# Performance work log

Measured on AMD Instinct MI355X. Metric: run time of the kernel, lower is better.

Reference implementation:

```python
import jax, jax.numpy as jnp
import numpy as np
from jax import lax

ALPHA = 1.0
BETA = 2.0
NUM_ANTS = 16384
NUM_NODES = 512
BATCH = 4096


def setup_inputs() -> dict:
    key = jax.random.key(0)
    k1, k2, k3 = jax.random.split(key, 3)
    x = jax.random.normal(k1, (BATCH, NUM_NODES), dtype=jnp.float32)
    # matches nn.Parameter(torch.ones(N,N)*0.1)
    pheromone_trails = jnp.ones((NUM_NODES, NUM_NODES), dtype=jnp.float32) * 0.1
    # matches nn.Parameter(torch.rand(N,N)*0.1)
    heuristic_info = jax.random.uniform(k2, (NUM_NODES, NUM_NODES), dtype=jnp.float32) * 0.1
    # matches register_buffer('ant_positions', randint(0, N, (num_ants,)))
    ant_positions = jax.random.randint(k3, (NUM_ANTS,), 0, NUM_NODES, dtype=jnp.int32)
    return {"x": x, "pheromone_trails": pheromone_trails,
            "heuristic_info": heuristic_info, "ant_positions": ant_positions}


def reference(x, pheromone_trails, heuristic_info, ant_positions):
    A, N = NUM_ANTS, NUM_NODES
    ant_ids = jnp.arange(A)

    # NOTE: the torch code's select_next_node always reads the row of the ant's
    # *initial* position (self.ant_positions is never updated inside forward),
    # so the unmasked scores are constant per ant. We replicate that faithfully.
    base = (pheromone_trails[ant_positions] ** ALPHA) * \
           (heuristic_info[ant_positions] ** BETA)          # [A, N]

    visited0 = jnp.zeros((A, N), dtype=bool).at[ant_ids, ant_positions].set(True)
    plen0 = jnp.zeros((A,), dtype=jnp.float32)

    def step(carry, _):
        key, visited, current, plen = carry
        key, sub = jax.random.split(key)
        # torch sets masked entries to 0 (NOT -inf) before softmax; replicate.
        logits = jnp.where(visited, 0.0, base)               # [A, N]
        # categorical == multinomial(softmax(logits), 1), vectorized over ants
        nxt = jax.random.categorical(sub, logits, axis=-1)   # [A] int
        plen = plen + heuristic_info[current, nxt]
        visited = visited.at[ant_ids, nxt].set(True)
        return (key, visited, nxt, plen), nxt

    carry0 = (jax.random.key(42), visited0, ant_positions.astype(jnp.int32), plen0)
    (_, _, _, path_lengths), sampled = lax.scan(step, carry0, None, length=N - 1)

    # full paths: [A, N] = start node followed by N-1 sampled nodes
    paths = jnp.concatenate([ant_positions[:, None].astype(sampled.dtype),
                             sampled.T], axis=1)
    # sequential 'if path_length < best' with strict < keeps the FIRST minimum,
    # which is exactly jnp.argmin
    best_idx = jnp.argmin(path_lengths)
    best_path = paths[best_idx].astype(jnp.float32)          # [N]
    return jnp.broadcast_to(best_path[None, :], (x.shape[0], N))
```

## Files before the change

### kernel.cpp

```cpp
#include <hip/hip_runtime.h>
#include <cstdint>
#include <cstddef>

#define A_NUM_ANTS   16384
#define N_NODES      512
#define N_STEPS      511
#define N_BATCH      4096

constexpr uint32_t rotl32(uint32_t x, int r) { return (x << r) | (x >> (32 - r)); }

constexpr void tf2x32(uint32_t k0, uint32_t k1, uint32_t x0, uint32_t x1,
                      uint32_t& o0, uint32_t& o1) {
  const uint32_t k2 = k0 ^ k1 ^ 0x1BD11BDAu;
  x0 += k0; x1 += k1;
  x0 += x1; x1 = rotl32(x1, 13); x1 ^= x0;
  x0 += x1; x1 = rotl32(x1, 15); x1 ^= x0;
  x0 += x1; x1 = rotl32(x1, 26); x1 ^= x0;
  x0 += x1; x1 = rotl32(x1,  6); x1 ^= x0;
  x0 += k1; x1 += k2 + 1u;
  x0 += x1; x1 = rotl32(x1, 17); x1 ^= x0;
  x0 += x1; x1 = rotl32(x1, 29); x1 ^= x0;
  x0 += x1; x1 = rotl32(x1, 16); x1 ^= x0;
  x0 += x1; x1 = rotl32(x1, 24); x1 ^= x0;
  x0 += k2; x1 += k0 + 2u;
  x0 += x1; x1 = rotl32(x1, 13); x1 ^= x0;
  x0 += x1; x1 = rotl32(x1, 15); x1 ^= x0;
  x0 += x1; x1 = rotl32(x1, 26); x1 ^= x0;
  x0 += x1; x1 = rotl32(x1,  6); x1 ^= x0;
  x0 += k0; x1 += k1 + 3u;
  x0 += x1; x1 = rotl32(x1, 17); x1 ^= x0;
  x0 += x1; x1 = rotl32(x1, 29); x1 ^= x0;
  x0 += x1; x1 = rotl32(x1, 16); x1 ^= x0;
  x0 += x1; x1 = rotl32(x1, 24); x1 ^= x0;
  x0 += k1; x1 += k2 + 4u;
  x0 += x1; x1 = rotl32(x1, 13); x1 ^= x0;
  x0 += x1; x1 = rotl32(x1, 15); x1 ^= x0;
  x0 += x1; x1 = rotl32(x1, 26); x1 ^= x0;
  x0 += x1; x1 = rotl32(x1,  6); x1 ^= x0;
  x0 += k2; x1 += k0 + 5u;
  o0 = x0; o1 = x1;
}

struct Subkeys { uint32_t k0[N_STEPS]; uint32_t k1[N_STEPS]; };

constexpr Subkeys make_subkeys() {
  Subkeys s{};
  uint32_t c0 = 0u, c1 = 42u;
  for (int t = 0; t < N_STEPS; ++t) {
    uint32_t n0 = 0, n1 = 0, s0 = 0, s1 = 0;
    tf2x32(c0, c1, 0u, 0u, n0, n1);
    tf2x32(c0, c1, 0u, 1u, s0, s1);
    s.k0[t] = s0; s.k1[t] = s1;
    c0 = n0; c1 = n1;
  }
  return s;
}

namespace { constexpr Subkeys H_SUBKEYS = make_subkeys(); }
__device__ __constant__ Subkeys SUBKEYS = H_SUBKEYS;

#define NEG_LN2   (-0.69314718056f)

template <bool WRITE_PATH>
__device__ __forceinline__ void simulate_ant(
    int a, int lane,
    const float* __restrict__ pher,
    const float* __restrict__ heur,
    int pos,
    float* __restrict__ plen_out,
    float* __restrict__ path_out)
{
  float    lm[8];
  uint32_t visited = 0;
  float    ebmin, ebmax;
  {
    const float* hrow = heur + (size_t)pos * N_NODES;
    const float* prow = pher + (size_t)pos * N_NODES;
    ebmin = 1.0f; ebmax = 1.0f;
#pragma unroll
    for (int q = 0; q < 8; ++q) {
      const int n = lane * 8 + q;
      const float hv = hrow[n];
      const float base = prow[n] * (hv * hv);
      const float eb = expf(-base);
      lm[q] = NEG_LN2 * eb;
      ebmin = fminf(ebmin, eb);
      ebmax = fmaxf(ebmax, eb);
      if (n == pos) visited |= (1u << q);
    }
  }

  int baddr[6];
#pragma unroll
  for (int r = 0; r < 6; ++r) baddr[r] = ((lane ^ (1 << r)) << 2);

#pragma unroll
  for (int r = 0; r < 6; ++r) {
    ebmin = fminf(ebmin, __int_as_float(
        __builtin_amdgcn_ds_bpermute(baddr[r], __float_as_int(ebmin))));
    ebmax = fmaxf(ebmax, __int_as_float(
        __builtin_amdgcn_ds_bpermute(baddr[r], __float_as_int(ebmax))));
  }
  const float allow = (ebmax / ebmin) * (1.0f + 2e-4f);

  int   cur  = pos;
  float plen = 0.0f;
  if (WRITE_PATH && lane == 0) path_out[0] = (float)pos;

  const uint32_t ctr_base = (uint32_t)(a * N_NODES + lane * 8);

  for (int t = 0; t < N_STEPS; ++t) {
    const uint32_t k0 = SUBKEYS.k0[t];
    const uint32_t k1 = SUBKEYS.k1[t];

    uint32_t m[8];
#pragma unroll
    for (int q = 0; q < 8; ++q) {
      uint32_t o0, o1;
      tf2x32(k0, k1, 0u, ctr_base + (uint32_t)q, o0, o1);
      m[q] = (o0 ^ o1) >> 9;
    }
    uint32_t mmax = m[0];
#pragma unroll
    for (int q = 1; q < 8; ++q) mmax = mmax > m[q] ? mmax : m[q];
#pragma unroll
    for (int r = 0; r < 6; ++r) {
      const uint32_t o = (uint32_t)__builtin_amdgcn_ds_bpermute(baddr[r], (int)mmax);
      mmax = mmax > o ? mmax : o;
    }
    const float L    = 23.0f - __log2f((float)mmax);
    const float uthr = __builtin_amdgcn_exp2f(-L * allow);
    const uint32_t mthr = (uint32_t)(uthr * 8388608.0f * (1.0f - 1e-4f));

    unsigned long long b[8];
    int tot = 0;
#pragma unroll
    for (int q = 0; q < 8; ++q) {
      b[q] = __ballot(m[q] >= mthr);
      tot += __popcll(b[q]);
    }

    int bn;
    if (tot == 1) {
      bn = 0;
#pragma unroll
      for (int q = 0; q < 8; ++q)
        if (b[q]) bn = (int)__builtin_ctzll(b[q]) * 8 + q;
    } else {
      float s[8];
#pragma unroll
      for (int q = 0; q < 8; ++q) {
        const float f  = __uint_as_float(m[q] | 0x3f800000u) - 1.0f;
        const float le = ((visited >> q) & 1u) ? NEG_LN2 : lm[q];
        s[q] = __log2f(f) * le;
      }
      float smin = s[0];
#pragma unroll
      for (int q = 1; q < 8; ++q) smin = fminf(smin, s[q]);
#pragma unroll
      for (int r = 0; r < 6; ++r)
        smin = fminf(smin, __int_as_float(
            __builtin_amdgcn_ds_bpermute(baddr[r], __float_as_int(smin))));
      int fq = 8;
#pragma unroll
      for (int q = 7; q >= 0; --q) if (s[q] == smin) fq = q;
      const unsigned long long mask = __ballot(fq < 8);
      const int winlane = __builtin_ctzll(mask);
      bn = __shfl(fq, winlane, 64) + winlane * 8;
    }

    if ((bn >> 3) == lane) visited |= (1u << (bn & 7));

    plen += heur[(size_t)cur * N_NODES + bn];
    cur = bn;
    if (WRITE_PATH && lane == 0) path_out[t + 1] = (float)bn;
  }

  if (!WRITE_PATH && lane == 0) plen_out[a] = plen;
}

__global__ __launch_bounds__(256, 6) void aco_sim_kernel(
    const float* __restrict__ pher, const float* __restrict__ heur,
    const int* __restrict__ pos0, float* __restrict__ plen_out, int num_ants)
{
  const int a = (int)((blockIdx.x * blockDim.x + threadIdx.x) >> 6);
  const int lane = threadIdx.x & 63;
  if (a >= num_ants) return;
  simulate_ant<false>(a, lane, pher, heur, pos0[a], plen_out, nullptr);
}

__global__ void aco_argmin_kernel(const float* __restrict__ plen,
                                  int* __restrict__ best, int num_ants) {
  const int tid = threadIdx.x;
  float bv = 3.4e38f;
  int   bi = 0;
  bool  have = false;
  for (int i = tid; i < num_ants; i += 256) {
    const float v = plen[i];
    if (!have || v < bv) { bv = v; bi = i; have = true; }
  }
#pragma unroll
  for (int off = 32; off >= 1; off >>= 1) {
    const float vo = __shfl_xor(bv, off, 64);
    const int   io = __shfl_xor(bi, off, 64);
    if (vo < bv || (vo == bv && io < bi)) { bv = vo; bi = io; }
  }
  __shared__ float sv[4];
  __shared__ int   si[4];
  const int w = tid >> 6;
  if ((tid & 63) == 0) { sv[w] = bv; si[w] = bi; }
  __syncthreads();
  if (tid == 0) {
    for (int j = 1; j < 4; ++j)
      if (sv[j] < bv || (sv[j] == bv && si[j] < bi)) { bv = sv[j]; bi = si[j]; }
    bi = bi < 0 ? 0 : (bi >= num_ants ? num_ants - 1 : bi);
    *best = bi;
  }
}

__global__ void aco_resim_kernel(const float* __restrict__ pher,
                                 const float* __restrict__ heur,
                                 const int* __restrict__ pos0,
                                 const int* __restrict__ best,
                                 float* __restrict__ path_out, int num_ants) {
  const int lane = threadIdx.x & 63;
  int a = *best;
  a = a < 0 ? 0 : (a >= num_ants ? num_ants - 1 : a);
  simulate_ant<true>(a, lane, pher, heur, pos0[a], nullptr, path_out);
}

__global__ void aco_bcast_kernel(float* __restrict__ out, int total4) {
  const int j = (int)(blockIdx.x * blockDim.x + threadIdx.x);
  if (j >= total4) return;
  const int row  = 1 + (j >> 7);
  const int col4 = j & 127;
  const float4 v = reinterpret_cast<const float4*>(out)[col4];
  reinterpret_cast<float4*>(out)[row * 128 + col4] = v;
}

extern "C" void kernel_launch(void* const* d_in, const int* in_sizes, int n_in,
                              void* d_out, int out_size, void* d_ws, size_t ws_size,
                              hipStream_t stream) {
  const float* pher = (const float*)d_in[1];
  const float* heur = (const float*)d_in[2];
  const int*   pos  = (const int*)d_in[3];
  float* out = (float*)d_out;
  const int num_ants = in_sizes[3];

  float* plen = out;
  int*   best = (int*)(out + A_NUM_ANTS);

  const int sim_blocks = (num_ants * 64 + 255) / 256;
  aco_sim_kernel<<<dim3(sim_blocks), dim3(256), 0, stream>>>(
      pher, heur, pos, plen, num_ants);
  aco_argmin_kernel<<<dim3(1), dim3(256), 0, stream>>>(plen, best, num_ants);
  aco_resim_kernel<<<dim3(1), dim3(64), 0, stream>>>(
      pher, heur, pos, best, out, num_ants);
  const int total4 = (out_size - N_NODES) / 4;
  aco_bcast_kernel<<<dim3((total4 + 255) / 256), dim3(256), 0, stream>>>(
      out, total4);
}
```

Measured before the change: 8.506 ms.

## Software-pipeline Threefry hashing and replace float threshold with integer math

```diff
diff --git a/kernel.cpp b/kernel.cpp
--- a/kernel.cpp
+++ b/kernel.cpp
@@ -61,6 +61,8 @@
 
 #define NEG_LN2   (-0.69314718056f)
 
+struct Frag { uint32_t m[8]; };
+
 template <bool WRITE_PATH>
 __device__ __forceinline__ void simulate_ant(
     int a, int lane,
@@ -101,7 +103,12 @@
     ebmax = fmaxf(ebmax, __int_as_float(
         __builtin_amdgcn_ds_bpermute(baddr[r], __float_as_int(ebmax))));
   }
-  const float allow = (ebmax / ebmin) * (1.0f + 2e-4f);
+  const float ratio = ebmax / ebmin;
+  const float delta = ratio * (1.0f + 3e-4f) - 1.0f + 1e-5f;
+  const float d15   = delta * 1.5f;
+  const bool  always_slow = !(d15 < 0.4f);
+  const uint32_t D32 = always_slow ? 0xFFFFFFFFu
+                     : ((uint32_t)(d15 * 4294967296.0f) + 1u);
 
   int   cur  = pos;
   float plen = 0.0f;
@@ -109,34 +116,41 @@
 
   const uint32_t ctr_base = (uint32_t)(a * N_NODES + lane * 8);
 
-  for (int t = 0; t < N_STEPS; ++t) {
+  auto hash8 = [&](Frag& f, int t) __attribute__((always_inline)) {
     const uint32_t k0 = SUBKEYS.k0[t];
     const uint32_t k1 = SUBKEYS.k1[t];
-
-    uint32_t m[8];
 #pragma unroll
     for (int q = 0; q < 8; ++q) {
       uint32_t o0, o1;
       tf2x32(k0, k1, 0u, ctr_base + (uint32_t)q, o0, o1);
-      m[q] = (o0 ^ o1) >> 9;
-    }
-    uint32_t mmax = m[0];
-#pragma unroll
-    for (int q = 1; q < 8; ++q) mmax = mmax > m[q] ? mmax : m[q];
+      f.m[q] = (o0 ^ o1) >> 9;
+    }
+  };
+
+  auto step = [&](Frag& use, Frag& pre, int t, int tpre, bool do_pre)
+      __attribute__((always_inline)) {
+    uint32_t mmax = use.m[0];
+#pragma unroll
+    for (int q = 1; q < 8; ++q) mmax = mmax > use.m[q] ? mmax : use.m[q];
 #pragma unroll
     for (int r = 0; r < 6; ++r) {
       const uint32_t o = (uint32_t)__builtin_amdgcn_ds_bpermute(baddr[r], (int)mmax);
       mmax = mmax > o ? mmax : o;
     }
-    const float L    = 23.0f - __log2f((float)mmax);
-    const float uthr = __builtin_amdgcn_exp2f(-L * allow);
-    const uint32_t mthr = (uint32_t)(uthr * 8388608.0f * (1.0f - 1e-4f));
+
+    if (do_pre) hash8(pre, tpre);
+
+    const uint32_t mmax_s = (uint32_t)__builtin_amdgcn_readfirstlane((int)mmax);
+    const uint32_t d   = 8388608u - mmax_s;
+    const uint32_t sub = __umulhi(D32, d) + 2u;
+    uint32_t mthr = mmax_s - sub;
+    if (always_slow || mmax_s < 4194304u) mthr = 0xFFFFFFFFu;
 
     unsigned long long b[8];
     int tot = 0;
 #pragma unroll
     for (int q = 0; q < 8; ++q) {
-      b[q] = __ballot(m[q] >= mthr);
+      b[q] = __ballot(use.m[q] >= mthr);
       tot += __popcll(b[q]);
     }
 
@@ -150,7 +164,7 @@
       float s[8];
 #pragma unroll
       for (int q = 0; q < 8; ++q) {
-        const float f  = __uint_as_float(m[q] | 0x3f800000u) - 1.0f;
+        const float f  = __uint_as_float(use.m[q] | 0x3f800000u) - 1.0f;
         const float le = ((visited >> q) & 1u) ? NEG_LN2 : lm[q];
         s[q] = __log2f(f) * le;
       }
@@ -174,7 +188,16 @@
     plen += heur[(size_t)cur * N_NODES + bn];
     cur = bn;
     if (WRITE_PATH && lane == 0) path_out[t + 1] = (float)bn;
-  }
+  };
+
+  Frag A, B;
+  hash8(A, 0);
+  for (int tt = 0; tt < (N_STEPS - 1) / 2; ++tt) {
+    const int t0 = 2 * tt;
+    step(A, B, t0,     t0 + 1, true);
+    step(B, A, t0 + 1, t0 + 2, true);
+  }
+  step(A, B, N_STEPS - 1, 0, false);
 
   if (!WRITE_PATH && lane == 0) plen_out[a] = plen;
 }
```

New measurement: 8.384 ms. No clear change (-1.4%).
